# Kernel optimization log

Measured on AMD Instinct MI355X. Metric: run time of the kernel, lower is better.

Reference implementation:

```python
import jax, jax.numpy as jnp
import numpy as np

# PairwiseChannelAdd(aggregation='max', mode='off-diag', source_axis=1)
# For each source channel k in [0, C-2]:
#   right = x[:, k+1:] + x[:, k];  left = x[:, :k+1] + x[:, k]
#   union of right+left covers ALL j in [0, C-1] (diagonal j==k included via `left`).
#   connec_k = max over (pair axis j, time axis T) of (x[:, j] + x[:, k])  -> [B, 1, F]
# stack over k -> [C-1, B, 1, F]; transpose([1,2,0,3]) -> [B, 1, C-1, F]

B, C, T, F = 8, 160, 512, 32

def setup_inputs() -> dict:
    key = jax.random.key(0)
    x = jax.random.normal(key, (B, C, T, F), dtype=jnp.float32)
    return {"x": x}

def reference(x):
    c = x.shape[1]
    ks = jnp.arange(c - 1)
    # lax.map keeps memory at one [B,C,T,F] pairwise-sum intermediate per step
    def per_k(k):
        # x[:, k] -> [B, T, F]; broadcast-add against all channels j -> [B, C, T, F]
        s = x + x[:, k][:, None, :, :]
        return jnp.max(s, axis=(1, 2))  # reduce over pair (j) and time -> [B, F]
    out = jax.lax.map(per_k, ks)        # [C-1, B, F]
    return jnp.transpose(out, (1, 0, 2))[:, None, :, :]  # [B, 1, C-1, F]
```

## Files before the change

### kernel.cpp

```cpp
#include <hip/hip_runtime.h>
#include <math.h>

#define B_DIM 8
#define C_DIM 160
#define T_DIM 512
#define F_DIM 32
#define F4 8
#define C1 159
#define TCH 8
#define NT (T_DIM / TCH)
#define NSUB 4
#define KPAD 17

__device__ __forceinline__ float4 fmax4(float4 a, float4 b) {
    return make_float4(fmaxf(a.x, b.x), fmaxf(a.y, b.y),
                       fmaxf(a.z, b.z), fmaxf(a.w, b.w));
}
__device__ __forceinline__ float4 fadd4(float4 a, float4 b) {
    return make_float4(a.x + b.x, a.y + b.y, a.z + b.z, a.w + b.w);
}
__device__ __forceinline__ float4 shfl_xor4(float4 v, int m) {
    return make_float4(__shfl_xor(v.x, m), __shfl_xor(v.y, m),
                       __shfl_xor(v.z, m), __shfl_xor(v.w, m));
}
#define NEG_INF4 make_float4(-INFINITY, -INFINITY, -INFINITY, -INFINITY)

__global__ __launch_bounds__(256)
void fused_kernel(const float* __restrict__ x, float* __restrict__ partial) {
    const int blk = blockIdx.x;
    const int b = blk >> 6;
    const int tc = blk & (NT - 1);
    const int t_base = tc * TCH;
    const int tid = threadIdx.x;
    const int f4 = tid & 7;
    const int eid = tid & 15;
    const int cg = tid >> 4;
    const int wave = tid >> 6;

    const float4* __restrict__ x4 = (const float4*)x;
    float4* __restrict__ p4 = (float4*)partial;

    __shared__ float4 Xlds[C_DIM * KPAD];
    __shared__ float4 redw[4 * 16];

    const int kg = tid >> 3;
    float4 accK[5];
    #pragma unroll
    for (int ki = 0; ki < 5; ++ki) accK[ki] = NEG_INF4;

    for (int s = 0; s < NSUB; ++s) {
        const int t0 = t_base + 2 * s;

        float4 macc = NEG_INF4;
        #pragma unroll
        for (int i = 0; i < 10; ++i) {
            const int c = cg + 16 * i;
            const float4 v = x4[((b * C_DIM + c) * T_DIM + t0) * F4 + eid];
            Xlds[c * KPAD + eid] = v;
            macc = fmax4(macc, v);
        }
        macc = fmax4(macc, shfl_xor4(macc, 16));
        macc = fmax4(macc, shfl_xor4(macc, 32));
        if ((tid & 63) < 16) redw[wave * 16 + eid] = macc;
        __syncthreads();

        float4 m0 = fmax4(fmax4(redw[f4],      redw[16 + f4]),
                          fmax4(redw[32 + f4], redw[48 + f4]));
        float4 m1 = fmax4(fmax4(redw[8 + f4],      redw[16 + 8 + f4]),
                          fmax4(redw[32 + 8 + f4], redw[48 + 8 + f4]));

        #pragma unroll
        for (int ki = 0; ki < 5; ++ki) {
            const int k = kg + 32 * ki;
            if (k < C1) {
                accK[ki] = fmax4(accK[ki],
                                 fadd4(Xlds[k * KPAD + f4], m0));
                accK[ki] = fmax4(accK[ki],
                                 fadd4(Xlds[k * KPAD + 8 + f4], m1));
            }
        }
        __syncthreads();
    }

    #pragma unroll
    for (int ki = 0; ki < 5; ++ki) {
        const int k = kg + 32 * ki;
        if (k < C1)
            p4[((b * C1 + k) * NT + tc) * F4 + f4] = accK[ki];
    }
}

__global__ __launch_bounds__(64)
void combine_kernel(const float* __restrict__ partial, float* __restrict__ out) {
    const int bk = blockIdx.x;
    const int lane = threadIdx.x;
    const float4* __restrict__ p = (const float4*)partial + bk * (NT * F4);

    float4 acc = NEG_INF4;
    #pragma unroll
    for (int j = 0; j < (NT * F4) / 64; ++j)
        acc = fmax4(acc, p[j * 64 + lane]);

    acc = fmax4(acc, shfl_xor4(acc, 8));
    acc = fmax4(acc, shfl_xor4(acc, 16));
    acc = fmax4(acc, shfl_xor4(acc, 32));
    if (lane < 8)
        ((float4*)out)[bk * F4 + lane] = acc;
}

extern "C" void kernel_launch(void* const* d_in, const int* in_sizes, int n_in,
                              void* d_out, int out_size, void* d_ws, size_t ws_size,
                              hipStream_t stream) {
    const float* x = (const float*)d_in[0];
    float* out = (float*)d_out;
    float* partial = (float*)d_ws;

    fused_kernel<<<B_DIM * NT, 256, 0, stream>>>(x, partial);
    combine_kernel<<<B_DIM * C1, 64, 0, stream>>>(partial, out);
}
```

Before: 120.7 us.

## Split into channel-max pass and per-channel pair max pass

Replaces the LDS-staged fused kernel and combine with two kernels. The first computes the max over channels for each (b,t,f), split into two channel halves. The second adds each channel k to that max and reduces over time. This removes the large per-(k,t-chunk) partial buffer and the LDS barriers, relying on max(x_j+x_k)=x_k+max_j x_j. In exchange x is read twice from global memory and the first pass has limited parallelism.

```diff
diff --git a/kernel.cpp b/kernel.cpp
--- a/kernel.cpp
+++ b/kernel.cpp
@@ -7,10 +7,10 @@
 #define F_DIM 32
 #define F4 8
 #define C1 159
-#define TCH 8
-#define NT (T_DIM / TCH)
-#define NSUB 4
-#define KPAD 17
+#define CSPLIT 2
+#define CCH (C_DIM / CSPLIT)
+#define TBLK 32
+#define NTB (T_DIM / TBLK)
 
 __device__ __forceinline__ float4 fmax4(float4 a, float4 b) {
     return make_float4(fmaxf(a.x, b.x), fmaxf(a.y, b.y),
@@ -26,86 +26,63 @@
 #define NEG_INF4 make_float4(-INFINITY, -INFINITY, -INFINITY, -INFINITY)
 
 __global__ __launch_bounds__(256)
-void fused_kernel(const float* __restrict__ x, float* __restrict__ partial) {
-    const int blk = blockIdx.x;
-    const int b = blk >> 6;
-    const int tc = blk & (NT - 1);
-    const int t_base = tc * TCH;
+void cmax_kernel(const float* __restrict__ x, float* __restrict__ mpart) {
+    const int bi = blockIdx.x;
+    const int tb = bi & (NTB - 1);
+    const int b  = (bi >> 4) & (B_DIM - 1);
+    const int cc = bi >> 7;
     const int tid = threadIdx.x;
     const int f4 = tid & 7;
-    const int eid = tid & 15;
-    const int cg = tid >> 4;
-    const int wave = tid >> 6;
+    const int t = tb * TBLK + (tid >> 3);
 
-    const float4* __restrict__ x4 = (const float4*)x;
-    float4* __restrict__ p4 = (float4*)partial;
+    const float4* __restrict__ x4 =
+        (const float4*)x + ((b * C_DIM + cc * CCH) * T_DIM + t) * F4 + f4;
 
-    __shared__ float4 Xlds[C_DIM * KPAD];
-    __shared__ float4 redw[4 * 16];
+    float4 acc = NEG_INF4;
+    #pragma unroll 8
+    for (int ci = 0; ci < CCH; ++ci)
+        acc = fmax4(acc, x4[ci * (T_DIM * F4)]);
 
-    const int kg = tid >> 3;
-    float4 accK[5];
-    #pragma unroll
-    for (int ki = 0; ki < 5; ++ki) accK[ki] = NEG_INF4;
-
-    for (int s = 0; s < NSUB; ++s) {
-        const int t0 = t_base + 2 * s;
-
-        float4 macc = NEG_INF4;
-        #pragma unroll
-        for (int i = 0; i < 10; ++i) {
-            const int c = cg + 16 * i;
-            const float4 v = x4[((b * C_DIM + c) * T_DIM + t0) * F4 + eid];
-            Xlds[c * KPAD + eid] = v;
-            macc = fmax4(macc, v);
-        }
-        macc = fmax4(macc, shfl_xor4(macc, 16));
-        macc = fmax4(macc, shfl_xor4(macc, 32));
-        if ((tid & 63) < 16) redw[wave * 16 + eid] = macc;
-        __syncthreads();
-
-        float4 m0 = fmax4(fmax4(redw[f4],      redw[16 + f4]),
-                          fmax4(redw[32 + f4], redw[48 + f4]));
-        float4 m1 = fmax4(fmax4(redw[8 + f4],      redw[16 + 8 + f4]),
-                          fmax4(redw[32 + 8 + f4], redw[48 + 8 + f4]));
-
-        #pragma unroll
-        for (int ki = 0; ki < 5; ++ki) {
-            const int k = kg + 32 * ki;
-            if (k < C1) {
-                accK[ki] = fmax4(accK[ki],
-                                 fadd4(Xlds[k * KPAD + f4], m0));
-                accK[ki] = fmax4(accK[ki],
-                                 fadd4(Xlds[k * KPAD + 8 + f4], m1));
-            }
-        }
-        __syncthreads();
-    }
-
-    #pragma unroll
-    for (int ki = 0; ki < 5; ++ki) {
-        const int k = kg + 32 * ki;
-        if (k < C1)
-            p4[((b * C1 + k) * NT + tc) * F4 + f4] = accK[ki];
-    }
+    ((float4*)mpart)[((cc * B_DIM + b) * T_DIM + t) * F4 + f4] = acc;
 }
 
-__global__ __launch_bounds__(64)
-void combine_kernel(const float* __restrict__ partial, float* __restrict__ out) {
-    const int bk = blockIdx.x;
-    const int lane = threadIdx.x;
-    const float4* __restrict__ p = (const float4*)partial + bk * (NT * F4);
+__global__ __launch_bounds__(256)
+void pair_kernel(const float* __restrict__ x, const float* __restrict__ mpart,
+                 float* __restrict__ out) {
+    const int bi = blockIdx.x;
+    const int b = bi / C1;
+    const int k = bi - b * C1;
+    const int tid = threadIdx.x;
+    const int f4 = tid & 7;
+    const int tsub = tid >> 3;
+
+    const float4* __restrict__ xk =
+        (const float4*)x + (b * C_DIM + k) * (T_DIM * F4);
+    const float4* __restrict__ m0 =
+        (const float4*)mpart + b * (T_DIM * F4);
+    const float4* __restrict__ m1 = m0 + B_DIM * (T_DIM * F4);
 
     float4 acc = NEG_INF4;
-    #pragma unroll
-    for (int j = 0; j < (NT * F4) / 64; ++j)
-        acc = fmax4(acc, p[j * 64 + lane]);
+    #pragma unroll 4
+    for (int it = 0; it < T_DIM / 32; ++it) {
+        const int idx = (it * 32 + tsub) * F4 + f4;
+        const float4 m = fmax4(m0[idx], m1[idx]);
+        acc = fmax4(acc, fadd4(xk[idx], m));
+    }
 
     acc = fmax4(acc, shfl_xor4(acc, 8));
     acc = fmax4(acc, shfl_xor4(acc, 16));
     acc = fmax4(acc, shfl_xor4(acc, 32));
-    if (lane < 8)
-        ((float4*)out)[bk * F4 + lane] = acc;
+
+    __shared__ float4 red[4][8];
+    const int wave = tid >> 6;
+    if ((tid & 63) < 8) red[wave][f4] = acc;
+    __syncthreads();
+    if (tid < 8) {
+        const float4 r = fmax4(fmax4(red[0][tid], red[1][tid]),
+                               fmax4(red[2][tid], red[3][tid]));
+        ((float4*)out)[(b * C1 + k) * F4 + tid] = r;
+    }
 }
 
 extern "C" void kernel_launch(void* const* d_in, const int* in_sizes, int n_in,
@@ -113,8 +90,8 @@
                               hipStream_t stream) {
     const float* x = (const float*)d_in[0];
     float* out = (float*)d_out;
-    float* partial = (float*)d_ws;
+    float* mpart = (float*)d_ws;
 
-    fused_kernel<<<B_DIM * NT, 256, 0, stream>>>(x, partial);
-    combine_kernel<<<B_DIM * C1, 64, 0, stream>>>(partial, out);
+    cmax_kernel<<<CSPLIT * B_DIM * NTB, 256, 0, stream>>>(x, mpart);
+    pair_kernel<<<B_DIM * C1, 256, 0, stream>>>(x, mpart, out);
 }
```

Result: slower. 128.4 us (+6.4%).
